# Optimization experiments

Hardware: AMD Instinct MI355X
Metric: run time of the kernel (lower is better)

Reference implementation:

```python
import jax, jax.numpy as jnp
import numpy as np

NUM_HEADS = 8
LN_EPS = 1e-5


def setup_inputs() -> dict:
    key = jax.random.key(0)
    k1, k2, k3 = jax.random.split(key, 3)
    B, N, C = 1, 4096, 256
    before = jax.random.normal(k1, (B, N, C), dtype=jnp.float32)
    after = jax.random.normal(k2, (B, N, C), dtype=jnp.float32)
    W_qkv = jax.random.normal(k3, (3 * C, C), dtype=jnp.float32) * (C ** -0.5)
    d = C // NUM_HEADS
    gamma = jnp.ones((d,), dtype=jnp.float32)
    beta = jnp.zeros((d,), dtype=jnp.float32)
    return {"before": before, "after": after, "W_qkv": W_qkv, "gamma": gamma, "beta": beta}


def _qkv_norm(x, W_qkv, gamma, beta, H):
    # x: [B,N,C] -> q,k,v each [B,H,N,d], LayerNorm over d applied to all of qkv
    B, N, C = x.shape
    d = C // H
    t = jnp.einsum('bnc,oc->bno', x, W_qkv)            # [B,N,3C]
    t = t.reshape(B, N, 3, H, d).transpose(2, 0, 3, 1, 4)  # [3,B,H,N,d]
    mu = jnp.mean(t, axis=-1, keepdims=True)
    var = jnp.mean(jnp.square(t - mu), axis=-1, keepdims=True)
    t = (t - mu) * jax.lax.rsqrt(var + LN_EPS) * gamma + beta
    return t[0], t[1], t[2]


def _cross_attn(q, k, v, scale):
    # q,k,v: [B,H,N,d] -> context [B,N,C]
    attn = jax.nn.softmax(jnp.einsum('bhqd,bhkd->bhqk', q, k) * scale, axis=-1)
    ctx = jnp.einsum('bhqk,bhkd->bhqd', attn, v)
    B, H, N, d = ctx.shape
    return ctx.transpose(0, 2, 1, 3).reshape(B, N, H * d)


def reference(before, after, W_qkv, gamma, beta):
    H = NUM_HEADS
    C = before.shape[-1]
    d = C // H
    scale = d ** -0.5
    q_b, k_b, v_b = _qkv_norm(before, W_qkv, gamma, beta, H)
    q_a, k_a, v_a = _qkv_norm(after, W_qkv, gamma, beta, H)
    context_a = _cross_attn(q_b, k_a, v_a, scale)  # before attends to after
    context_b = _cross_attn(q_a, k_b, v_b, scale)  # after attends to before
    return (context_b, context_a)
```

## Files before the change

kernel.cpp:

```cpp
#include <hip/hip_runtime.h>


typedef __attribute__((ext_vector_type(8))) short short8;
typedef __attribute__((ext_vector_type(4))) float float4v;
typedef __attribute__((ext_vector_type(2))) unsigned int uint2v;

#define NTOK 4096
#define CDIM 256
#define HEADS 8
#define DHEAD 32

#define QOFF 0
#define KOFF (2*HEADS*NTOK*DHEAD)
#define VOFF (2*(2*HEADS*NTOK*DHEAD))
#define WOFF (3*(2*HEADS*NTOK*DHEAD))

__device__ inline unsigned short f2bf(float f) {
    union { float f; unsigned u; } v; v.f = f;
    unsigned r = v.u + 0x7FFFu + ((v.u >> 16) & 1u);
    return (unsigned short)(r >> 16);
}

__global__ __launch_bounds__(256) void wconv_kernel(
    const float* __restrict__ W, unsigned short* __restrict__ ws)
{
    int idx = blockIdx.x*256 + threadIdx.x;
    int R = idx >> 5, oct = idx & 31;
    int C = oct * 8;
    const float4* p = reinterpret_cast<const float4*>(W + R*CDIM + C);
    float4 a = p[0], b = p[1];
    short8 f;
    f[0]=(short)f2bf(a.x); f[1]=(short)f2bf(a.y); f[2]=(short)f2bf(a.z); f[3]=(short)f2bf(a.w);
    f[4]=(short)f2bf(b.x); f[5]=(short)f2bf(b.y); f[6]=(short)f2bf(b.z); f[7]=(short)f2bf(b.w);
    int o32 = R >> 5, r = R & 31;
    int kk = C >> 5, quad = (C >> 3) & 3;
    int dst = o32*8192 + (kk*2 + (r>>4))*512 + (quad*16 + (r&15))*8;
    *reinterpret_cast<short8*>(ws + WOFF + dst) = f;
}

__global__ __launch_bounds__(256) void qkv_ln_kernel(
    const float* __restrict__ before, const float* __restrict__ after,
    const float* __restrict__ gamma, const float* __restrict__ beta,
    unsigned short* __restrict__ ws)
{
    const int tid  = threadIdx.x;
    const int lane = tid & 63;
    const int w    = tid >> 6;
    const int quad = lane >> 4;
    const int l16  = lane & 15;
    const int rt   = blockIdx.x >> 3;
    const int oq   = blockIdx.x & 7;

    const int mrow_frag = rt*64 + w*16 + l16;
    const int inp_f = mrow_frag >> 12;
    const int n_f   = mrow_frag & 4095;
    const float* x = inp_f ? after : before;

    short8 afrag[8];
#pragma unroll
    for (int kk = 0; kk < 8; kk++) {
        const float4* p = reinterpret_cast<const float4*>(x + n_f*CDIM + kk*32 + quad*8);
        float4 a = p[0], b = p[1];
        short8 f;
        f[0]=(short)f2bf(a.x); f[1]=(short)f2bf(a.y); f[2]=(short)f2bf(a.z); f[3]=(short)f2bf(a.w);
        f[4]=(short)f2bf(b.x); f[5]=(short)f2bf(b.y); f[6]=(short)f2bf(b.z); f[7]=(short)f2bf(b.w);
        afrag[kk] = f;
    }

    const float g0  = gamma[l16], g1  = gamma[16+l16];
    const float be0 = beta[l16],  be1 = beta[16+l16];
    const float cscale = 0.17677669529663687f * 1.4426950408889634f;

    const int mrow_out  = rt*64 + w*16 + quad*4;
    const int inp_o     = mrow_out >> 12;
    const int n_o_base  = mrow_out & 4095;

    const unsigned short* wbf = ws + WOFF;

    for (int o32 = oq*3; o32 < oq*3 + 3; o32++) {
        const unsigned short* wb = wbf + o32*8192 + lane*8;
        float4v acc0 = {0.f,0.f,0.f,0.f}, acc1 = {0.f,0.f,0.f,0.f};
#pragma unroll
        for (int kk = 0; kk < 8; kk++) {
            short8 b0 = *reinterpret_cast<const short8*>(wb + (kk*2    )*512);
            short8 b1 = *reinterpret_cast<const short8*>(wb + (kk*2 + 1)*512);
            acc0 = __builtin_amdgcn_mfma_f32_16x16x32_bf16(afrag[kk], b0, acc0, 0,0,0);
            acc1 = __builtin_amdgcn_mfma_f32_16x16x32_bf16(afrag[kk], b1, acc1, 0,0,0);
        }

        const int which = o32 >> 3;
        const int h     = o32 & 7;
        unsigned short* qk = ws + (which == 0 ? QOFF : KOFF) + ((inp_o*HEADS + h)*NTOK)*DHEAD;
        unsigned short* vt = ws + VOFF + ((inp_o*HEADS + h)*DHEAD)*NTOK;
        const float qs = (which == 0) ? cscale : 1.0f;

#pragma unroll
        for (int i = 0; i < 4; i++) {
            float sum = acc0[i] + acc1[i];
            float sq  = acc0[i]*acc0[i] + acc1[i]*acc1[i];
#pragma unroll
            for (int m = 1; m < 16; m <<= 1) {
                sum += __shfl_xor(sum, m);
                sq  += __shfl_xor(sq,  m);
            }
            float mu   = sum * (1.0f/32.0f);
            float var  = sq * (1.0f/32.0f) - mu*mu;
            float rstd = rsqrtf(var + 1e-5f);
            float v0 = ((acc0[i]-mu)*rstd*g0 + be0) * qs;
            float v1 = ((acc1[i]-mu)*rstd*g1 + be1) * qs;
            int n = n_o_base + i;
            if (which < 2) {
                qk[n*DHEAD + l16]      = f2bf(v0);
                qk[n*DHEAD + 16 + l16] = f2bf(v1);
            } else {
                int kb = n >> 6, ki = n & 63;
                int kp2 = kb*64 + (ki & 15)*4 + (ki >> 4);
                vt[l16*NTOK + kp2]       = f2bf(v0);
                vt[(16+l16)*NTOK + kp2]  = f2bf(v1);
            }
        }
    }
}

__global__ __launch_bounds__(256, 4) void attn_kernel(
    const unsigned short* __restrict__ ws, float* __restrict__ out)
{
    __shared__ unsigned short vlds[2][32*136];
    __shared__ unsigned short plds[4][32*72];

    const int X  = blockIdx.z;
    const int h  = blockIdx.y;
    const int qb = blockIdx.x;
    const int qinp = 1 - X, kvinp = X;
    const int tid  = threadIdx.x;
    const int lane = tid & 63;
    const int w    = tid >> 6;
    const int qh   = w & 1;
    const int kh   = w >> 1;
    const int quad = lane >> 4;
    const int l16  = lane & 15;

    const unsigned short* qbase = ws + QOFF + ((qinp*HEADS + h)*NTOK)*DHEAD;
    const unsigned short* kbase = ws + KOFF + ((kvinp*HEADS + h)*NTOK)*DHEAD;
    const unsigned short* vbase = ws + VOFF + ((kvinp*HEADS + h)*DHEAD)*NTOK;

    const int q0 = qb*64 + qh*32;
    const short8 qf0 = *reinterpret_cast<const short8*>(qbase + (q0 + l16)*DHEAD      + quad*8);
    const short8 qf1 = *reinterpret_cast<const short8*>(qbase + (q0 + 16 + l16)*DHEAD + quad*8);

    const unsigned short* kp   = kbase + (kh*2048 + l16)*DHEAD + quad*8;
    const unsigned short* vsrc = vbase + kh*2048;

    float4v O00 = {0,0,0,0}, O01 = {0,0,0,0}, O10 = {0,0,0,0}, O11 = {0,0,0,0};
    float rs[2][4];
#pragma unroll
    for (int s = 0; s < 2; s++)
#pragma unroll
        for (int i = 0; i < 4; i++) rs[s][i] = 0.f;

    unsigned short* pw  = plds[w];
    unsigned short* vh  = vlds[kh];
    const int t2 = qh*64 + lane;

    for (int j = 0; j < 16; j++) {
        __syncthreads();
#pragma unroll
        for (int r = 0; r < 4; r++) {
            int c = t2 + 128*r;
            short8 d = *reinterpret_cast<const short8*>(vsrc + (c>>4)*NTOK + j*128 + (c&15)*8);
            *reinterpret_cast<short8*>(vh + (c>>4)*136 + (c&15)*8) = d;
        }
        __syncthreads();

#pragma unroll
        for (int c = 0; c < 2; c++) {
            float4v S0[4], S1[4];
#pragma unroll
            for (int t = 0; t < 4; t++) {
                short8 kf = *reinterpret_cast<const short8*>(kp + (j*128 + c*64 + t*16)*DHEAD);
                float4v z = {0,0,0,0};
                S0[t] = __builtin_amdgcn_mfma_f32_16x16x32_bf16(qf0, kf, z, 0,0,0);
                S1[t] = __builtin_amdgcn_mfma_f32_16x16x32_bf16(qf1, kf, z, 0,0,0);
            }
#pragma unroll
            for (int s = 0; s < 2; s++) {
#pragma unroll
                for (int i = 0; i < 4; i++) {
                    uint2v wv;
#pragma unroll
                    for (int t4 = 0; t4 < 2; t4++) {
                        float pa = __builtin_amdgcn_exp2f(s ? S1[2*t4][i]   : S0[2*t4][i]);
                        float pb = __builtin_amdgcn_exp2f(s ? S1[2*t4+1][i] : S0[2*t4+1][i]);
                        rs[s][i] += pa + pb;
                        union { float f; unsigned u; } ua, ub;
                        ua.f = pa; ub.f = pb;
                        wv[t4] = __builtin_amdgcn_perm(ub.u + 0x8000u, ua.u + 0x8000u,
                                                       0x07060302u);
                    }
                    *reinterpret_cast<uint2v*>(pw + (s*16 + quad*4 + i)*72 + l16*4) = wv;
                }
            }
#pragma unroll
            for (int kk = 0; kk < 2; kk++) {
                short8 p0 = *reinterpret_cast<const short8*>(pw + l16*72      + kk*32 + quad*8);
                short8 p1 = *reinterpret_cast<const short8*>(pw + (16+l16)*72 + kk*32 + quad*8);
                short8 v0 = *reinterpret_cast<const short8*>(vh + l16*136      + c*64 + kk*32 + quad*8);
                short8 v1 = *reinterpret_cast<const short8*>(vh + (16+l16)*136 + c*64 + kk*32 + quad*8);
                O00 = __builtin_amdgcn_mfma_f32_16x16x32_bf16(p0, v0, O00, 0,0,0);
                O01 = __builtin_amdgcn_mfma_f32_16x16x32_bf16(p0, v1, O01, 0,0,0);
                O10 = __builtin_amdgcn_mfma_f32_16x16x32_bf16(p1, v0, O10, 0,0,0);
                O11 = __builtin_amdgcn_mfma_f32_16x16x32_bf16(p1, v1, O11, 0,0,0);
            }
        }
    }

    float lsum[2][4];
#pragma unroll
    for (int s = 0; s < 2; s++)
#pragma unroll
        for (int i = 0; i < 4; i++) {
            float l = rs[s][i];
#pragma unroll
            for (int m = 1; m < 16; m <<= 1) l += __shfl_xor(l, m);
            lsum[s][i] = l;
        }

    __syncthreads();

    float* comb = reinterpret_cast<float*>(&plds[0][0]) + qh*(32*34);
    if (kh == 1) {
#pragma unroll
        for (int s = 0; s < 2; s++)
#pragma unroll
            for (int i = 0; i < 4; i++) {
                int row = s*16 + quad*4 + i;
                comb[row*34 + l16]      = (s ? O10[i] : O00[i]);
                comb[row*34 + 16 + l16] = (s ? O11[i] : O01[i]);
                if (l16 == 0) comb[row*34 + 32] = lsum[s][i];
            }
    }
    __syncthreads();

    if (kh == 0) {
        float* ob = out + (size_t)X*NTOK*CDIM + h*DHEAD;
#pragma unroll
        for (int s = 0; s < 2; s++) {
#pragma unroll
            for (int i = 0; i < 4; i++) {
                int row = s*16 + quad*4 + i;
                float l = lsum[s][i] + comb[row*34 + 32];
                float inv = 1.0f / l;
                float a = ((s ? O10[i] : O00[i]) + comb[row*34 + l16])      * inv;
                float b = ((s ? O11[i] : O01[i]) + comb[row*34 + 16 + l16]) * inv;
                int orow = q0 + row;
                ob[orow*CDIM + l16]      = a;
                ob[orow*CDIM + 16 + l16] = b;
            }
        }
    }
}

extern "C" void kernel_launch(void* const* d_in, const int* in_sizes, int n_in,
                              void* d_out, int out_size, void* d_ws, size_t ws_size,
                              hipStream_t stream)
{
    const float* before = (const float*)d_in[0];
    const float* after  = (const float*)d_in[1];
    const float* W      = (const float*)d_in[2];
    const float* gamma  = (const float*)d_in[3];
    const float* beta   = (const float*)d_in[4];
    float* out          = (float*)d_out;
    unsigned short* ws  = (unsigned short*)d_ws;

    hipLaunchKernelGGL(wconv_kernel, dim3(96), dim3(256), 0, stream, W, ws);
    hipLaunchKernelGGL(qkv_ln_kernel, dim3(1024), dim3(256), 0, stream,
                       before, after, gamma, beta, ws);
    hipLaunchKernelGGL(attn_kernel, dim3(64, 8, 2), dim3(256), 0, stream, ws, out);
}
```

Before: 162.2 us.

## Keep softmax probabilities in registers via transposed QK MFMA, drop P LDS round-trip

Computes S transposed (K as the A operand, Q as B), so each lane's exp'd scores already sit in the register layout the PV MFMA needs as its A operand. The per-wave P buffer in shared memory and its store/load round-trip are removed. The V transpose layout in the projection kernel changes to 32-key groups with a matching slot permutation. Row sums are now reduced across quads and redistributed by shuffles at the end. The risk is a mismatch between the new V slot permutation and the register P ordering, which would make the output wrong.

```diff
diff --git a/kernel.cpp b/kernel.cpp
--- a/kernel.cpp
+++ b/kernel.cpp
@@ -3,7 +3,7 @@
 
 typedef __attribute__((ext_vector_type(8))) short short8;
 typedef __attribute__((ext_vector_type(4))) float float4v;
-typedef __attribute__((ext_vector_type(2))) unsigned int uint2v;
+typedef __attribute__((ext_vector_type(4))) unsigned int uint4v;
 
 #define NTOK 4096
 #define CDIM 256
@@ -113,8 +113,9 @@
                 qk[n*DHEAD + l16]      = f2bf(v0);
                 qk[n*DHEAD + 16 + l16] = f2bf(v1);
             } else {
-                int kb = n >> 6, ki = n & 63;
-                int kp2 = kb*64 + (ki & 15)*4 + (ki >> 4);
+                int kb = n >> 5, ki = n & 31;
+                int slot = ((ki & 15) >> 2)*8 + (ki & 3) + ((ki >> 4) << 2);
+                int kp2 = kb*32 + slot;
                 vt[l16*NTOK + kp2]       = f2bf(v0);
                 vt[(16+l16)*NTOK + kp2]  = f2bf(v1);
             }
@@ -126,7 +127,6 @@
     const unsigned short* __restrict__ ws, float* __restrict__ out)
 {
     __shared__ unsigned short vlds[2][32*136];
-    __shared__ unsigned short plds[4][32*72];
 
     const int X  = blockIdx.z;
     const int h  = blockIdx.y;
@@ -152,14 +152,9 @@
     const unsigned short* vsrc = vbase + kh*2048;
 
     float4v O00 = {0,0,0,0}, O01 = {0,0,0,0}, O10 = {0,0,0,0}, O11 = {0,0,0,0};
-    float rs[2][4];
-#pragma unroll
-    for (int s = 0; s < 2; s++)
-#pragma unroll
-        for (int i = 0; i < 4; i++) rs[s][i] = 0.f;
-
-    unsigned short* pw  = plds[w];
-    unsigned short* vh  = vlds[kh];
+    float rs0 = 0.f, rs1 = 0.f;
+
+    unsigned short* vh = vlds[kh];
     const int t2 = qh*64 + lane;
 
     for (int j = 0; j < 16; j++) {
@@ -173,61 +168,57 @@
         __syncthreads();
 
 #pragma unroll
-        for (int c = 0; c < 2; c++) {
-            float4v S0[4], S1[4];
-#pragma unroll
-            for (int t = 0; t < 4; t++) {
-                short8 kf = *reinterpret_cast<const short8*>(kp + (j*128 + c*64 + t*16)*DHEAD);
+        for (int grp = 0; grp < 4; grp++) {
+            short8 kf0 = *reinterpret_cast<const short8*>(kp + (j*128 + grp*32     )*DHEAD);
+            short8 kf1 = *reinterpret_cast<const short8*>(kp + (j*128 + grp*32 + 16)*DHEAD);
+            short8 v0  = *reinterpret_cast<const short8*>(vh + l16*136      + grp*32 + quad*8);
+            short8 v1  = *reinterpret_cast<const short8*>(vh + (16+l16)*136 + grp*32 + quad*8);
+#pragma unroll
+            for (int s = 0; s < 2; s++) {
+                const short8 qf = s ? qf1 : qf0;
                 float4v z = {0,0,0,0};
-                S0[t] = __builtin_amdgcn_mfma_f32_16x16x32_bf16(qf0, kf, z, 0,0,0);
-                S1[t] = __builtin_amdgcn_mfma_f32_16x16x32_bf16(qf1, kf, z, 0,0,0);
-            }
-#pragma unroll
-            for (int s = 0; s < 2; s++) {
-#pragma unroll
-                for (int i = 0; i < 4; i++) {
-                    uint2v wv;
-#pragma unroll
-                    for (int t4 = 0; t4 < 2; t4++) {
-                        float pa = __builtin_amdgcn_exp2f(s ? S1[2*t4][i]   : S0[2*t4][i]);
-                        float pb = __builtin_amdgcn_exp2f(s ? S1[2*t4+1][i] : S0[2*t4+1][i]);
-                        rs[s][i] += pa + pb;
-                        union { float f; unsigned u; } ua, ub;
-                        ua.f = pa; ub.f = pb;
-                        wv[t4] = __builtin_amdgcn_perm(ub.u + 0x8000u, ua.u + 0x8000u,
-                                                       0x07060302u);
-                    }
-                    *reinterpret_cast<uint2v*>(pw + (s*16 + quad*4 + i)*72 + l16*4) = wv;
+                float4v S0 = __builtin_amdgcn_mfma_f32_16x16x32_bf16(kf0, qf, z, 0,0,0);
+                float4v S1 = __builtin_amdgcn_mfma_f32_16x16x32_bf16(kf1, qf, z, 0,0,0);
+                float e0 = __builtin_amdgcn_exp2f(S0[0]);
+                float e1 = __builtin_amdgcn_exp2f(S0[1]);
+                float e2 = __builtin_amdgcn_exp2f(S0[2]);
+                float e3 = __builtin_amdgcn_exp2f(S0[3]);
+                float e4 = __builtin_amdgcn_exp2f(S1[0]);
+                float e5 = __builtin_amdgcn_exp2f(S1[1]);
+                float e6 = __builtin_amdgcn_exp2f(S1[2]);
+                float e7 = __builtin_amdgcn_exp2f(S1[3]);
+                float rsum = ((e0+e1)+(e2+e3)) + ((e4+e5)+(e6+e7));
+                if (s) rs1 += rsum; else rs0 += rsum;
+                union { float f; unsigned u; } u0,u1,u2,u3,u4,u5,u6,u7;
+                u0.f=e0; u1.f=e1; u2.f=e2; u3.f=e3; u4.f=e4; u5.f=e5; u6.f=e6; u7.f=e7;
+                union { short8 s8; uint4v u4v; } pf;
+                pf.u4v[0] = __builtin_amdgcn_perm(u1.u + 0x8000u, u0.u + 0x8000u, 0x07060302u);
+                pf.u4v[1] = __builtin_amdgcn_perm(u3.u + 0x8000u, u2.u + 0x8000u, 0x07060302u);
+                pf.u4v[2] = __builtin_amdgcn_perm(u5.u + 0x8000u, u4.u + 0x8000u, 0x07060302u);
+                pf.u4v[3] = __builtin_amdgcn_perm(u7.u + 0x8000u, u6.u + 0x8000u, 0x07060302u);
+                if (s == 0) {
+                    O00 = __builtin_amdgcn_mfma_f32_16x16x32_bf16(pf.s8, v0, O00, 0,0,0);
+                    O01 = __builtin_amdgcn_mfma_f32_16x16x32_bf16(pf.s8, v1, O01, 0,0,0);
+                } else {
+                    O10 = __builtin_amdgcn_mfma_f32_16x16x32_bf16(pf.s8, v0, O10, 0,0,0);
+                    O11 = __builtin_amdgcn_mfma_f32_16x16x32_bf16(pf.s8, v1, O11, 0,0,0);
                 }
             }
-#pragma unroll
-            for (int kk = 0; kk < 2; kk++) {
-                short8 p0 = *reinterpret_cast<const short8*>(pw + l16*72      + kk*32 + quad*8);
-                short8 p1 = *reinterpret_cast<const short8*>(pw + (16+l16)*72 + kk*32 + quad*8);
-                short8 v0 = *reinterpret_cast<const short8*>(vh + l16*136      + c*64 + kk*32 + quad*8);
-                short8 v1 = *reinterpret_cast<const short8*>(vh + (16+l16)*136 + c*64 + kk*32 + quad*8);
-                O00 = __builtin_amdgcn_mfma_f32_16x16x32_bf16(p0, v0, O00, 0,0,0);
-                O01 = __builtin_amdgcn_mfma_f32_16x16x32_bf16(p0, v1, O01, 0,0,0);
-                O10 = __builtin_amdgcn_mfma_f32_16x16x32_bf16(p1, v0, O10, 0,0,0);
-                O11 = __builtin_amdgcn_mfma_f32_16x16x32_bf16(p1, v1, O11, 0,0,0);
-            }
-        }
-    }
-
-    float lsum[2][4];
-#pragma unroll
-    for (int s = 0; s < 2; s++)
-#pragma unroll
-        for (int i = 0; i < 4; i++) {
-            float l = rs[s][i];
-#pragma unroll
-            for (int m = 1; m < 16; m <<= 1) l += __shfl_xor(l, m);
-            lsum[s][i] = l;
-        }
+        }
+    }
+
+    float ls0 = rs0; ls0 += __shfl_xor(ls0, 16); ls0 += __shfl_xor(ls0, 32);
+    float ls1 = rs1; ls1 += __shfl_xor(ls1, 16); ls1 += __shfl_xor(ls1, 32);
+    float lrow[2][4];
+#pragma unroll
+    for (int i = 0; i < 4; i++) {
+        lrow[0][i] = __shfl(ls0, quad*4 + i);
+        lrow[1][i] = __shfl(ls1, quad*4 + i);
+    }
 
     __syncthreads();
 
-    float* comb = reinterpret_cast<float*>(&plds[0][0]) + qh*(32*34);
+    float* comb = reinterpret_cast<float*>(&vlds[0][0]) + qh*(32*34);
     if (kh == 1) {
 #pragma unroll
         for (int s = 0; s < 2; s++)
@@ -236,7 +227,7 @@
                 int row = s*16 + quad*4 + i;
                 comb[row*34 + l16]      = (s ? O10[i] : O00[i]);
                 comb[row*34 + 16 + l16] = (s ? O11[i] : O01[i]);
-                if (l16 == 0) comb[row*34 + 32] = lsum[s][i];
+                if (l16 == 0) comb[row*34 + 32] = lrow[s][i];
             }
     }
     __syncthreads();
@@ -248,7 +239,7 @@
 #pragma unroll
             for (int i = 0; i < 4; i++) {
                 int row = s*16 + quad*4 + i;
-                float l = lsum[s][i] + comb[row*34 + 32];
+                float l = lrow[s][i] + comb[row*34 + 32];
                 float inv = 1.0f / l;
                 float a = ((s ? O10[i] : O00[i]) + comb[row*34 + l16])      * inv;
                 float b = ((s ? O11[i] : O01[i]) + comb[row*34 + 16 + l16]) * inv;
```

Measured after the change: 154.1 us. -5.0%, faster.
